# Optimization experiments

Hardware: AMD Instinct MI355X
Metric: run time of the kernel (lower is better)

The kernel has to match this reference:

```python
import jax, jax.numpy as jnp
import numpy as np

B, T, V, H = 2048, 48, 59, 512


def _uniform(key, shape, fan_in):
    stdv = 1.0 / np.sqrt(fan_in)
    return jax.random.uniform(key, shape, jnp.float32, -stdv, stdv)


def setup_inputs() -> dict:
    key = jax.random.key(0)
    ks = jax.random.split(key, 24)
    x = jax.random.normal(ks[0], (B, T, V), jnp.float32)
    mask = (jax.random.uniform(ks[1], (B, T, V)) < 0.8).astype(jnp.float32)
    deltas = jax.random.uniform(ks[2], (B, T, V), jnp.float32)
    return {
        "x": x, "mask": mask, "deltas": deltas,
        # Decay h (temp_decay_h): W [H,V], b [H]
        "W_gh": _uniform(ks[3], (H, V), V), "b_gh": _uniform(ks[4], (H,), V),
        # Decay x (diag): only diagonal of [V,V] is used -> store diag [V]
        "w_gx": _uniform(ks[5], (V,), V), "b_gx": _uniform(ks[6], (V,), V),
        # hist: Linear(H -> V)
        "W_hist": _uniform(ks[7], (V, H), H), "b_hist": _uniform(ks[8], (V,), H),
        "W_fr": _uniform(ks[9], (V, V), V), "b_fr": _uniform(ks[10], (V,), V),
        # weight_combine: Linear(2V -> V)
        "W_wc": _uniform(ks[11], (V, 2 * V), 2 * V), "b_wc": _uniform(ks[12], (V,), 2 * V),
        # LSTMCell(2V -> H), torch gate order i,f,g,o
        "W_ih": _uniform(ks[13], (4 * H, 2 * V), 2 * V),
        "W_hh": _uniform(ks[14], (4 * H, H), H),
        "b_ih": _uniform(ks[15], (4 * H,), H),
        "b_hh": _uniform(ks[16], (4 * H,), H),
    }


def _rits_forward(x, mask, deltas, W_gh, b_gh, w_gx, b_gx, W_hist, b_hist,
                  W_fr, b_fr, W_wc, b_wc, W_ih, W_hh, b_ih, b_hh):
    Bb, Tt, Vv = x.shape
    Hh = W_gh.shape[0]
    offdiag = 1.0 - jnp.eye(Vv, dtype=x.dtype)
    W_fr_m = W_fr * offdiag

    def step(carry, inp):
        h, c, loss = carry
        x_t, m_t, d_t = inp  # each [B, V]
        # temporal decay of hidden state
        gamma_h = jnp.exp(-jax.nn.relu(d_t @ W_gh.T + b_gh))  # [B, H]
        h = h * gamma_h
        # history-based estimate
        x_h = h @ W_hist.T + b_hist  # [B, V]
        x_r = m_t * x_t + (1.0 - m_t) * x_h
        xu = x_r @ W_fr_m.T + b_fr  # [B, V]
        # diagonal input decay
        gamma_x = jnp.exp(-jax.nn.relu(d_t * w_gx + b_gx))  # [B, V]
        # combination weights (note: no sigmoid, faithful to source)
        beta = jnp.concatenate([gamma_x, m_t], axis=-1) @ W_wc.T + b_wc  # [B, V]
        x_comb = beta * xu + (1.0 - beta) * x_h
        loss = loss + jnp.sum(jnp.abs(x_t - x_comb) * m_t) / (jnp.sum(m_t) + 1e-5)
        x_imp_t = m_t * x_t + (1.0 - m_t) * x_comb
        # LSTM cell
        inp_t = jnp.concatenate([x_imp_t, m_t], axis=-1)  # [B, 2V]
        gates = inp_t @ W_ih.T + b_ih + h @ W_hh.T + b_hh  # [B, 4H]
        i_g, f_g, g_g, o_g = jnp.split(gates, 4, axis=-1)
        c = jax.nn.sigmoid(f_g) * c + jax.nn.sigmoid(i_g) * jnp.tanh(g_g)
        h = jax.nn.sigmoid(o_g) * jnp.tanh(c)
        return (h, c, loss), (x_imp_t, h)

    h0 = jnp.zeros((Bb, Hh), x.dtype)
    c0 = jnp.zeros((Bb, Hh), x.dtype)
    loss0 = jnp.zeros((), x.dtype)
    xs = (jnp.swapaxes(x, 0, 1), jnp.swapaxes(mask, 0, 1), jnp.swapaxes(deltas, 0, 1))
    (h, c, x_loss), (x_imp_t, hiddens_t) = jax.lax.scan(step, (h0, c0, loss0), xs)
    x_imp = jnp.swapaxes(x_imp_t, 0, 1)      # [B, T, V]
    hiddens = jnp.swapaxes(hiddens_t, 0, 1)  # [B, T, H]
    return x_imp, x_loss, hiddens


def reference(x, mask, deltas, W_gh, b_gh, w_gx, b_gx, W_hist, b_hist,
              W_fr, b_fr, W_wc, b_wc, W_ih, W_hh, b_ih, b_hh):
    return _rits_forward(x, mask, deltas, W_gh, b_gh, w_gx, b_gx, W_hist, b_hist,
                         W_fr, b_fr, W_wc, b_wc, W_ih, W_hh, b_ih, b_hh)
```

## Files before the change

### kernel.cpp

```cpp
#include <hip/hip_runtime.h>

#define B_ 2048
#define T_ 48
#define V_ 59
#define H_ 512
#define KP_ 640
#define G4_ 2048

typedef __bf16 bf16x8 __attribute__((ext_vector_type(8)));
typedef float f32x4 __attribute__((ext_vector_type(4)));

__device__ __forceinline__ unsigned short f2bf(float x){
  union { float f; unsigned u; } v; v.f = x;
  unsigned r = (v.u + 0x7FFFu + ((v.u >> 16) & 1u)) >> 16;
  return (unsigned short)r;
}
__device__ __forceinline__ float sigf(float x){ return 1.f/(1.f+expf(-x)); }

static const size_t OFF_Hws = 0;
static const size_t OFF_Cws = 4194304;
static const size_t OFF_LN  = 8388608;
static const size_t OFF_LD  = OFF_LN + 256;
static const size_t MEMSET_BYTES = OFF_LN + 512;
static const size_t OFF_A   = OFF_LN + 512;
static const size_t OFF_WGT = OFF_A  + (size_t)B_*KP_*2;
static const size_t OFF_WGH = OFF_WGT + (size_t)G4_*KP_*2;
static const size_t OFF_WHB = OFF_WGH + 120832;
static const size_t OFF_WFR = OFF_WHB + 120832;
static const size_t OFF_WWC = OFF_WFR + 14080;

__global__ void init_k(const float* __restrict__ W_gh, const float* __restrict__ W_hist,
                       const float* __restrict__ W_fr, const float* __restrict__ W_wc,
                       const float* __restrict__ W_ih, const float* __restrict__ W_hh,
                       float* __restrict__ WghT, unsigned short* __restrict__ WhB,
                       float* __restrict__ WfrT, float* __restrict__ WwcT,
                       unsigned short* __restrict__ WgT, unsigned short* __restrict__ A_buf)
{
  int tid = blockIdx.x*blockDim.x + threadIdx.x;
  int nt  = gridDim.x*blockDim.x;
  for (int i = tid; i < V_*H_; i += nt){ int v = i >> 9, j = i & 511; WghT[i] = W_gh[j*V_ + v]; }
  for (int i = tid; i < 64*H_; i += nt){ int n = i >> 9; WhB[i] = (n < V_) ? f2bf(W_hist[i]) : (unsigned short)0; }
  for (int i = tid; i < V_*V_; i += nt){ int u = i / V_, v = i - u*V_; WfrT[i] = (u==v) ? 0.f : W_fr[v*V_ + u]; }
  for (int i = tid; i < 2*V_*V_; i += nt){ int u = i / V_, v = i - u*V_; WwcT[i] = W_wc[v*(2*V_) + u]; }
  for (int i = tid; i < G4_*KP_; i += nt){
    int n = i / KP_, k = i - n*KP_;
    float v = 0.f;
    if (k < 2*V_)      v = W_ih[n*(2*V_) + k];
    else if (k < 630)  v = W_hh[n*H_ + (k-118)];
    WgT[i] = f2bf(v);
  }
  for (int i = tid; i < B_*10; i += nt){ int b = i / 10, p = i - b*10; A_buf[(size_t)b*KP_ + 630 + p] = 0; }
}

__global__ __launch_bounds__(512) void phase1(int t,
    const float* __restrict__ x, const float* __restrict__ mk, const float* __restrict__ dl,
    const float* __restrict__ b_gh, const float* __restrict__ w_gx, const float* __restrict__ b_gx,
    const float* __restrict__ b_hist, const float* __restrict__ b_fr, const float* __restrict__ b_wc,
    const float* __restrict__ WghT, const unsigned short* __restrict__ WhB,
    const float* __restrict__ WfrT, const float* __restrict__ WwcT,
    const float* __restrict__ h_ws, unsigned short* __restrict__ A_buf,
    float* __restrict__ out_ximp, float* __restrict__ loss_num, float* __restrict__ loss_den)
{
  __shared__ float d_s[8*64], m_s[8*64], x_s[8*64];
  __shared__ float xh_s[8*64], xr_s[8*64], gx_s[8*64];
  __shared__ unsigned short hA[16*520];
  __shared__ float red[16];
  const int tid = threadIdx.x;
  const int r1  = blockIdx.x * 8;

  if (tid < 8*V_) {
    int b = tid / V_, v = tid - b*V_;
    size_t g = ((size_t)(r1+b)*T_ + t)*V_ + v;
    d_s[b*64+v] = dl[g];
    m_s[b*64+v] = mk[g];
    x_s[b*64+v] = x[g];
  }
  __syncthreads();

  {
    int j = tid;
    float acc[8];
#pragma unroll
    for (int b=0;b<8;++b) acc[b]=0.f;
    for (int v=0; v<V_; ++v) {
      float wv = WghT[v*H_ + j];
#pragma unroll
      for (int b=0;b<8;++b) acc[b] += d_s[b*64+v]*wv;
    }
    float bg = b_gh[j];
#pragma unroll
    for (int b=0;b<8;++b) {
      float gh = expf(-fmaxf(acc[b]+bg, 0.f));
      float hv = h_ws[(size_t)(r1+b)*H_ + j] * gh;
      unsigned short hb = f2bf(hv);
      hA[b*520 + j] = hb;
      A_buf[(size_t)(r1+b)*KP_ + 118 + j] = hb;
    }
  }
  __syncthreads();

  if (tid < 256) {
    const int w = tid >> 6, lane = tid & 63, col = lane & 15, quad = lane >> 4;
    f32x4 acc = (f32x4)(0.f);
    const unsigned short* wb = WhB + (size_t)(w*16 + col)*H_;
#pragma unroll
    for (int kk = 0; kk < 16; ++kk) {
      bf16x8 a  = *reinterpret_cast<const bf16x8*>(&hA[col*520 + kk*32 + quad*8]);
      bf16x8 bb = *reinterpret_cast<const bf16x8*>(wb + kk*32 + quad*8);
      acc = __builtin_amdgcn_mfma_f32_16x16x32_bf16(a, bb, acc, 0, 0, 0);
    }
    if (quad < 2) {
      int v = w*16 + col;
      float bh = (v < V_) ? b_hist[v] : 0.f;
#pragma unroll
      for (int r=0; r<4; ++r) xh_s[(quad*4+r)*64 + v] = acc[r] + bh;
    }
  } else {
    for (int i = tid - 256; i < 512; i += 256) {
      int b = i >> 6, v = i & 63;
      if (v < V_) {
        float mm = m_s[b*64+v], dd = d_s[b*64+v];
        gx_s[b*64+v] = expf(-fmaxf(dd*w_gx[v]+b_gx[v], 0.f));
        A_buf[(size_t)(r1+b)*KP_ + V_ + v] = f2bf(mm);
      }
    }
  }
  __syncthreads();

  {
    int b = tid>>6, v = tid&63;
    if (v < V_) {
      float mm = m_s[b*64+v];
      xr_s[b*64+v] = mm*x_s[b*64+v] + (1.f-mm)*xh_s[b*64+v];
    }
  }
  __syncthreads();

  float num = 0.f, den = 0.f;
  {
    int b = tid>>6, v = tid&63;
    if (v < V_) {
      float xu = b_fr[v], bt = b_wc[v];
      for (int u=0; u<V_; ++u) {
        xu += xr_s[b*64+u]*WfrT[u*V_+v];
        bt += gx_s[b*64+u]*WwcT[u*V_+v] + m_s[b*64+u]*WwcT[(V_+u)*V_+v];
      }
      float xh = xh_s[b*64+v];
      float xc = bt*xu + (1.f-bt)*xh;
      float mm = m_s[b*64+v], xx = x_s[b*64+v];
      num = fabsf(xx - xc)*mm;
      den = mm;
      float xi = mm*xx + (1.f-mm)*xc;
      out_ximp[((size_t)(r1+b)*T_ + t)*V_ + v] = xi;
      A_buf[(size_t)(r1+b)*KP_ + v] = f2bf(xi);
    }
  }
#pragma unroll
  for (int off=32; off; off>>=1){ num += __shfl_down(num, off); den += __shfl_down(den, off); }
  int wid = tid>>6, lane = tid&63;
  if (lane == 0){ red[wid] = num; red[8+wid] = den; }
  __syncthreads();
  if (tid == 0){
    float n=0.f, d=0.f;
    for (int i=0;i<8;++i){ n += red[i]; d += red[8+i]; }
    atomicAdd(&loss_num[t], n);
    atomicAdd(&loss_den[t], d);
  }
}

__global__ __launch_bounds__(512) void phase2(int t,
    const unsigned short* __restrict__ A_buf, const unsigned short* __restrict__ WgT,
    const float* __restrict__ b_ih, const float* __restrict__ b_hh,
    float* __restrict__ h_ws, float* __restrict__ c_ws, float* __restrict__ out_hid)
{
  __shared__ uint4 ldsA[128*8];
  __shared__ uint4 ldsB[128*8];
  const int tid  = threadIdx.x;
  const int r0   = blockIdx.x * 128;
  const int j0   = blockIdx.y * 32;
  const int w    = tid >> 6;
  const int rg   = w >> 1;
  const int uh   = w & 1;
  const int lane = tid & 63;
  const int col  = lane & 15;
  const int quad = lane >> 4;

  f32x4 acc[2][4];
#pragma unroll
  for (int i=0;i<2;++i)
#pragma unroll
    for (int g=0;g<4;++g) acc[i][g] = (f32x4)(0.f);

  for (int s = 0; s < 10; ++s) {
#pragma unroll
    for (int p=0; p<2; ++p) {
      int idx = p*512 + tid;
      int r = idx >> 3, c = idx & 7;
      ldsA[r*8 + (c ^ (r&7))] = *reinterpret_cast<const uint4*>(A_buf + (size_t)(r0+r)*KP_ + s*64 + c*8);
      int ng = ((r>>5)<<9) + j0 + (r&31);
      ldsB[r*8 + (c ^ (r&7))] = *reinterpret_cast<const uint4*>(WgT + (size_t)ng*KP_ + s*64 + c*8);
    }
    __syncthreads();
#pragma unroll
    for (int kk=0; kk<2; ++kk) {
      bf16x8 af[2], bfr[4];
#pragma unroll
      for (int mf=0; mf<2; ++mf) {
        int r = rg*32 + mf*16 + col;
        af[mf] = *reinterpret_cast<const bf16x8*>(&ldsA[r*8 + ((kk*4+quad) ^ (r&7))]);
      }
#pragma unroll
      for (int g=0; g<4; ++g) {
        int r = g*32 + uh*16 + col;
        bfr[g] = *reinterpret_cast<const bf16x8*>(&ldsB[r*8 + ((kk*4+quad) ^ (r&7))]);
      }
#pragma unroll
      for (int mf=0; mf<2; ++mf)
#pragma unroll
        for (int g=0; g<4; ++g)
          acc[mf][g] = __builtin_amdgcn_mfma_f32_16x16x32_bf16(af[mf], bfr[g], acc[mf][g], 0, 0, 0);
    }
    __syncthreads();
  }

  {
    int u = j0 + uh*16 + col;
    float bi  = b_ih[u]        + b_hh[u];
    float bf_ = b_ih[H_+u]     + b_hh[H_+u];
    float bg  = b_ih[2*H_+u]   + b_hh[2*H_+u];
    float bo  = b_ih[3*H_+u]   + b_hh[3*H_+u];
#pragma unroll
    for (int mf=0; mf<2; ++mf) {
#pragma unroll
      for (int r=0; r<4; ++r) {
        int b = r0 + rg*32 + mf*16 + quad*4 + r;
        float gi = acc[mf][0][r] + bi;
        float gf = acc[mf][1][r] + bf_;
        float gg = acc[mf][2][r] + bg;
        float go = acc[mf][3][r] + bo;
        size_t idx = (size_t)b*H_ + u;
        float co = c_ws[idx];
        float cn = sigf(gf)*co + sigf(gi)*tanhf(gg);
        float hn = sigf(go)*tanhf(cn);
        c_ws[idx] = cn;
        h_ws[idx] = hn;
        out_hid[((size_t)b*T_ + t)*H_ + u] = hn;
      }
    }
  }
}

__global__ void loss_k(const float* __restrict__ loss_num, const float* __restrict__ loss_den,
                       float* __restrict__ out_loss)
{
  int tid = threadIdx.x;
  float v = 0.f;
  if (tid < T_) v = loss_num[tid]/(loss_den[tid] + 1e-5f);
#pragma unroll
  for (int off=32; off; off>>=1) v += __shfl_down(v, off);
  if (tid == 0) *out_loss = v;
}

extern "C" void kernel_launch(void* const* d_in, const int* in_sizes, int n_in,
                              void* d_out, int out_size, void* d_ws, size_t ws_size,
                              hipStream_t stream)
{
  const float* x      = (const float*)d_in[0];
  const float* mk     = (const float*)d_in[1];
  const float* dl     = (const float*)d_in[2];
  const float* W_gh   = (const float*)d_in[3];
  const float* b_gh   = (const float*)d_in[4];
  const float* w_gx   = (const float*)d_in[5];
  const float* b_gx   = (const float*)d_in[6];
  const float* W_hist = (const float*)d_in[7];
  const float* b_hist = (const float*)d_in[8];
  const float* W_fr   = (const float*)d_in[9];
  const float* b_fr   = (const float*)d_in[10];
  const float* W_wc   = (const float*)d_in[11];
  const float* b_wc   = (const float*)d_in[12];
  const float* W_ih   = (const float*)d_in[13];
  const float* W_hh   = (const float*)d_in[14];
  const float* b_ih   = (const float*)d_in[15];
  const float* b_hh   = (const float*)d_in[16];

  char* ws = (char*)d_ws;
  float*          h_ws   = (float*)(ws + OFF_Hws);
  float*          c_ws   = (float*)(ws + OFF_Cws);
  float*          lnum   = (float*)(ws + OFF_LN);
  float*          lden   = (float*)(ws + OFF_LD);
  unsigned short* A_buf  = (unsigned short*)(ws + OFF_A);
  unsigned short* WgT    = (unsigned short*)(ws + OFF_WGT);
  float*          WghT   = (float*)(ws + OFF_WGH);
  unsigned short* WhB    = (unsigned short*)(ws + OFF_WHB);
  float*          WfrT   = (float*)(ws + OFF_WFR);
  float*          WwcT   = (float*)(ws + OFF_WWC);

  float* out      = (float*)d_out;
  float* out_ximp = out;
  float* out_loss = out + (size_t)B_*T_*V_;
  float* out_hid  = out + (size_t)B_*T_*V_ + 1;

  hipMemsetAsync(d_ws, 0, MEMSET_BYTES, stream);
  init_k<<<1024, 256, 0, stream>>>(W_gh, W_hist, W_fr, W_wc, W_ih, W_hh,
                                   WghT, WhB, WfrT, WwcT, WgT, A_buf);
  for (int t = 0; t < T_; ++t) {
    phase1<<<256, 512, 0, stream>>>(t, x, mk, dl, b_gh, w_gx, b_gx, b_hist, b_fr, b_wc,
                                    WghT, WhB, WfrT, WwcT, h_ws, A_buf,
                                    out_ximp, lnum, lden);
    phase2<<<dim3(16,16), 512, 0, stream>>>(t, A_buf, WgT, b_ih, b_hh,
                                            h_ws, c_ws, out_hid);
  }
  loss_k<<<1, 64, 0, stream>>>(lnum, lden, out_loss);
}
```

Before: 2.363 ms.

## Fuse per-step kernels into one persistent kernel with grid barriers; precompute beta

Replaces the 96 per-timestep kernel launches with a single persistent kernel of 256 blocks. The blocks synchronise through an atomic-counter grid barrier between the input-imputation phase and the LSTM GEMM phase. The cell state now stays in registers instead of global memory. The weight-combine beta term, which does not depend on the recurrence, is computed for all timesteps up front in a separate parallel kernel, along with the loss denominators. The design relies on all 256 blocks being resident at once, and spin barriers add their own latency in exchange for removing launch overhead.

Measured after the change: 5.006 ms. 112% more time.

```diff
diff --git a/kernel.cpp b/kernel.cpp
--- a/kernel.cpp
+++ b/kernel.cpp
@@ -6,6 +6,7 @@
 #define H_ 512
 #define KP_ 640
 #define G4_ 2048
+#define NBLK_ 256
 
 typedef __bf16 bf16x8 __attribute__((ext_vector_type(8)));
 typedef float f32x4 __attribute__((ext_vector_type(4)));
@@ -17,23 +18,23 @@
 }
 __device__ __forceinline__ float sigf(float x){ return 1.f/(1.f+expf(-x)); }
 
-static const size_t OFF_Hws = 0;
-static const size_t OFF_Cws = 4194304;
-static const size_t OFF_LN  = 8388608;
-static const size_t OFF_LD  = OFF_LN + 256;
-static const size_t MEMSET_BYTES = OFF_LN + 512;
-static const size_t OFF_A   = OFF_LN + 512;
-static const size_t OFF_WGT = OFF_A  + (size_t)B_*KP_*2;
-static const size_t OFF_WGH = OFF_WGT + (size_t)G4_*KP_*2;
-static const size_t OFF_WHB = OFF_WGH + 120832;
-static const size_t OFF_WFR = OFF_WHB + 120832;
-static const size_t OFF_WWC = OFF_WFR + 14080;
+static const size_t OFF_H    = 0;
+static const size_t OFF_LN   = 4194304;
+static const size_t OFF_LD   = OFF_LN + 256;
+static const size_t OFF_CNT  = OFF_LD + 256;
+static const size_t MEMSET_BYTES = OFF_CNT + 256;
+static const size_t OFF_A    = MEMSET_BYTES;
+static const size_t OFF_WGT  = OFF_A + (size_t)B_*KP_*2;
+static const size_t OFF_WGH  = OFF_WGT + (size_t)G4_*KP_*2;
+static const size_t OFF_WHB  = OFF_WGH + 120832;
+static const size_t OFF_WFR  = OFF_WHB + 65536;
+static const size_t OFF_BETA = OFF_WFR + 14080;
 
 __global__ void init_k(const float* __restrict__ W_gh, const float* __restrict__ W_hist,
-                       const float* __restrict__ W_fr, const float* __restrict__ W_wc,
+                       const float* __restrict__ W_fr,
                        const float* __restrict__ W_ih, const float* __restrict__ W_hh,
                        float* __restrict__ WghT, unsigned short* __restrict__ WhB,
-                       float* __restrict__ WfrT, float* __restrict__ WwcT,
+                       float* __restrict__ WfrT,
                        unsigned short* __restrict__ WgT, unsigned short* __restrict__ A_buf)
 {
   int tid = blockIdx.x*blockDim.x + threadIdx.x;
@@ -41,7 +42,6 @@
   for (int i = tid; i < V_*H_; i += nt){ int v = i >> 9, j = i & 511; WghT[i] = W_gh[j*V_ + v]; }
   for (int i = tid; i < 64*H_; i += nt){ int n = i >> 9; WhB[i] = (n < V_) ? f2bf(W_hist[i]) : (unsigned short)0; }
   for (int i = tid; i < V_*V_; i += nt){ int u = i / V_, v = i - u*V_; WfrT[i] = (u==v) ? 0.f : W_fr[v*V_ + u]; }
-  for (int i = tid; i < 2*V_*V_; i += nt){ int u = i / V_, v = i - u*V_; WwcT[i] = W_wc[v*(2*V_) + u]; }
   for (int i = tid; i < G4_*KP_; i += nt){
     int n = i / KP_, k = i - n*KP_;
     float v = 0.f;
@@ -52,213 +52,258 @@
   for (int i = tid; i < B_*10; i += nt){ int b = i / 10, p = i - b*10; A_buf[(size_t)b*KP_ + 630 + p] = 0; }
 }
 
-__global__ __launch_bounds__(512) void phase1(int t,
+__global__ __launch_bounds__(256) void beta_k(
+    const float* __restrict__ mk, const float* __restrict__ dl,
+    const float* __restrict__ w_gx, const float* __restrict__ b_gx,
+    const float* __restrict__ W_wc, const float* __restrict__ b_wc,
+    float* __restrict__ beta_pre, float* __restrict__ loss_den)
+{
+  __shared__ float gx[4][64], mm[4][64];
+  const int tid = threadIdx.x;
+  const int rw  = tid >> 6, v = tid & 63;
+  const int row = blockIdx.x*4 + rw;
+  size_t base = (size_t)row * V_;
+  float m = 0.f, g = 0.f;
+  if (v < V_){
+    float d = dl[base+v];
+    m = mk[base+v];
+    g = expf(-fmaxf(d*w_gx[v]+b_gx[v], 0.f));
+  }
+  gx[rw][v] = g; mm[rw][v] = m;
+  __syncthreads();
+  if (v < V_){
+    float bt = b_wc[v];
+    const float* wr = W_wc + (size_t)v*(2*V_);
+    for (int u = 0; u < V_; ++u)
+      bt += gx[rw][u]*wr[u] + mm[rw][u]*wr[V_+u];
+    beta_pre[base+v] = bt;
+  }
+  float s = m;
+#pragma unroll
+  for (int off=32; off; off>>=1) s += __shfl_down(s, off);
+  if (v == 0){
+    int t = row % T_;
+    atomicAdd(&loss_den[t], s);
+  }
+}
+
+__device__ __forceinline__ void grid_bar(unsigned int* cnt, unsigned int target){
+  __syncthreads();
+  if (threadIdx.x == 0){
+    __threadfence();
+    __hip_atomic_fetch_add(cnt, 1u, __ATOMIC_RELEASE, __HIP_MEMORY_SCOPE_AGENT);
+    while (__hip_atomic_load(cnt, __ATOMIC_RELAXED, __HIP_MEMORY_SCOPE_AGENT) < target)
+      __builtin_amdgcn_s_sleep(1);
+    __threadfence();
+  }
+  __syncthreads();
+}
+
+__global__ __launch_bounds__(512) void fused(
     const float* __restrict__ x, const float* __restrict__ mk, const float* __restrict__ dl,
-    const float* __restrict__ b_gh, const float* __restrict__ w_gx, const float* __restrict__ b_gx,
-    const float* __restrict__ b_hist, const float* __restrict__ b_fr, const float* __restrict__ b_wc,
+    const float* __restrict__ b_gh, const float* __restrict__ b_hist, const float* __restrict__ b_fr,
     const float* __restrict__ WghT, const unsigned short* __restrict__ WhB,
-    const float* __restrict__ WfrT, const float* __restrict__ WwcT,
-    const float* __restrict__ h_ws, unsigned short* __restrict__ A_buf,
-    float* __restrict__ out_ximp, float* __restrict__ loss_num, float* __restrict__ loss_den)
+    const float* __restrict__ WfrT, const float* __restrict__ beta_pre,
+    const unsigned short* __restrict__ WgT,
+    const float* __restrict__ b_ih, const float* __restrict__ b_hh,
+    float* h_ws, unsigned short* A_buf, unsigned int* bar_cnt,
+    float* loss_num, const float* __restrict__ loss_den,
+    float* __restrict__ out_ximp, float* __restrict__ out_hid, float* __restrict__ out_loss)
 {
-  __shared__ float d_s[8*64], m_s[8*64], x_s[8*64];
-  __shared__ float xh_s[8*64], xr_s[8*64], gx_s[8*64];
-  __shared__ unsigned short hA[16*520];
-  __shared__ float red[16];
-  const int tid = threadIdx.x;
-  const int r1  = blockIdx.x * 8;
-
-  if (tid < 8*V_) {
-    int b = tid / V_, v = tid - b*V_;
-    size_t g = ((size_t)(r1+b)*T_ + t)*V_ + v;
-    d_s[b*64+v] = dl[g];
-    m_s[b*64+v] = mk[g];
-    x_s[b*64+v] = x[g];
-  }
-  __syncthreads();
-
-  {
-    int j = tid;
-    float acc[8];
-#pragma unroll
-    for (int b=0;b<8;++b) acc[b]=0.f;
-    for (int v=0; v<V_; ++v) {
-      float wv = WghT[v*H_ + j];
-#pragma unroll
-      for (int b=0;b<8;++b) acc[b] += d_s[b*64+v]*wv;
-    }
-    float bg = b_gh[j];
-#pragma unroll
-    for (int b=0;b<8;++b) {
-      float gh = expf(-fmaxf(acc[b]+bg, 0.f));
-      float hv = h_ws[(size_t)(r1+b)*H_ + j] * gh;
-      unsigned short hb = f2bf(hv);
-      hA[b*520 + j] = hb;
-      A_buf[(size_t)(r1+b)*KP_ + 118 + j] = hb;
-    }
-  }
-  __syncthreads();
-
-  if (tid < 256) {
-    const int w = tid >> 6, lane = tid & 63, col = lane & 15, quad = lane >> 4;
-    f32x4 acc = (f32x4)(0.f);
-    const unsigned short* wb = WhB + (size_t)(w*16 + col)*H_;
-#pragma unroll
-    for (int kk = 0; kk < 16; ++kk) {
-      bf16x8 a  = *reinterpret_cast<const bf16x8*>(&hA[col*520 + kk*32 + quad*8]);
-      bf16x8 bb = *reinterpret_cast<const bf16x8*>(wb + kk*32 + quad*8);
-      acc = __builtin_amdgcn_mfma_f32_16x16x32_bf16(a, bb, acc, 0, 0, 0);
-    }
-    if (quad < 2) {
-      int v = w*16 + col;
-      float bh = (v < V_) ? b_hist[v] : 0.f;
-#pragma unroll
-      for (int r=0; r<4; ++r) xh_s[(quad*4+r)*64 + v] = acc[r] + bh;
-    }
-  } else {
-    for (int i = tid - 256; i < 512; i += 256) {
-      int b = i >> 6, v = i & 63;
-      if (v < V_) {
-        float mm = m_s[b*64+v], dd = d_s[b*64+v];
-        gx_s[b*64+v] = expf(-fmaxf(dd*w_gx[v]+b_gx[v], 0.f));
-        A_buf[(size_t)(r1+b)*KP_ + V_ + v] = f2bf(mm);
-      }
-    }
-  }
-  __syncthreads();
-
-  {
-    int b = tid>>6, v = tid&63;
-    if (v < V_) {
-      float mm = m_s[b*64+v];
-      xr_s[b*64+v] = mm*x_s[b*64+v] + (1.f-mm)*xh_s[b*64+v];
-    }
-  }
-  __syncthreads();
-
-  float num = 0.f, den = 0.f;
-  {
-    int b = tid>>6, v = tid&63;
-    if (v < V_) {
-      float xu = b_fr[v], bt = b_wc[v];
-      for (int u=0; u<V_; ++u) {
-        xu += xr_s[b*64+u]*WfrT[u*V_+v];
-        bt += gx_s[b*64+u]*WwcT[u*V_+v] + m_s[b*64+u]*WwcT[(V_+u)*V_+v];
-      }
-      float xh = xh_s[b*64+v];
-      float xc = bt*xu + (1.f-bt)*xh;
-      float mm = m_s[b*64+v], xx = x_s[b*64+v];
-      num = fabsf(xx - xc)*mm;
-      den = mm;
-      float xi = mm*xx + (1.f-mm)*xc;
-      out_ximp[((size_t)(r1+b)*T_ + t)*V_ + v] = xi;
-      A_buf[(size_t)(r1+b)*KP_ + v] = f2bf(xi);
-    }
-  }
-#pragma unroll
-  for (int off=32; off; off>>=1){ num += __shfl_down(num, off); den += __shfl_down(den, off); }
-  int wid = tid>>6, lane = tid&63;
-  if (lane == 0){ red[wid] = num; red[8+wid] = den; }
-  __syncthreads();
-  if (tid == 0){
-    float n=0.f, d=0.f;
-    for (int i=0;i<8;++i){ n += red[i]; d += red[8+i]; }
-    atomicAdd(&loss_num[t], n);
-    atomicAdd(&loss_den[t], d);
-  }
-}
-
-__global__ __launch_bounds__(512) void phase2(int t,
-    const unsigned short* __restrict__ A_buf, const unsigned short* __restrict__ WgT,
-    const float* __restrict__ b_ih, const float* __restrict__ b_hh,
-    float* __restrict__ h_ws, float* __restrict__ c_ws, float* __restrict__ out_hid)
-{
-  __shared__ uint4 ldsA[128*8];
-  __shared__ uint4 ldsB[128*8];
+  __shared__ union {
+    struct {
+      float d_s[512], m_s[512], x_s[512], xh_s[512], xr_s[512];
+      unsigned short hA[16*520];
+      float red[8];
+    } p1;
+    struct { uint4 sA[1024]; uint4 sB[1024]; } p2;
+  } sm;
+
   const int tid  = threadIdx.x;
-  const int r0   = blockIdx.x * 128;
-  const int j0   = blockIdx.y * 32;
-  const int w    = tid >> 6;
-  const int rg   = w >> 1;
-  const int uh   = w & 1;
+  const int blk  = blockIdx.x;
+  const int r1   = blk * 8;
+  const int r0   = (blk & 15) * 128;
+  const int j0   = (blk >> 4) * 32;
+  const int wid  = tid >> 6;
   const int lane = tid & 63;
   const int col  = lane & 15;
   const int quad = lane >> 4;
-
-  f32x4 acc[2][4];
+  const int rg   = wid >> 1;
+  const int uh   = wid & 1;
+
+  const int u2 = j0 + uh*16 + col;
+  const float bi  = b_ih[u2]      + b_hh[u2];
+  const float bfg = b_ih[H_+u2]   + b_hh[H_+u2];
+  const float bgg = b_ih[2*H_+u2] + b_hh[2*H_+u2];
+  const float bog = b_ih[3*H_+u2] + b_hh[3*H_+u2];
+  const float bgj = b_gh[tid];
+
+  float creg[2][4];
 #pragma unroll
   for (int i=0;i<2;++i)
 #pragma unroll
-    for (int g=0;g<4;++g) acc[i][g] = (f32x4)(0.f);
-
-  for (int s = 0; s < 10; ++s) {
-#pragma unroll
-    for (int p=0; p<2; ++p) {
-      int idx = p*512 + tid;
-      int r = idx >> 3, c = idx & 7;
-      ldsA[r*8 + (c ^ (r&7))] = *reinterpret_cast<const uint4*>(A_buf + (size_t)(r0+r)*KP_ + s*64 + c*8);
-      int ng = ((r>>5)<<9) + j0 + (r&31);
-      ldsB[r*8 + (c ^ (r&7))] = *reinterpret_cast<const uint4*>(WgT + (size_t)ng*KP_ + s*64 + c*8);
-    }
-    __syncthreads();
-#pragma unroll
-    for (int kk=0; kk<2; ++kk) {
-      bf16x8 af[2], bfr[4];
-#pragma unroll
-      for (int mf=0; mf<2; ++mf) {
-        int r = rg*32 + mf*16 + col;
-        af[mf] = *reinterpret_cast<const bf16x8*>(&ldsA[r*8 + ((kk*4+quad) ^ (r&7))]);
-      }
-#pragma unroll
-      for (int g=0; g<4; ++g) {
-        int r = g*32 + uh*16 + col;
-        bfr[g] = *reinterpret_cast<const bf16x8*>(&ldsB[r*8 + ((kk*4+quad) ^ (r&7))]);
-      }
-#pragma unroll
-      for (int mf=0; mf<2; ++mf)
-#pragma unroll
-        for (int g=0; g<4; ++g)
-          acc[mf][g] = __builtin_amdgcn_mfma_f32_16x16x32_bf16(af[mf], bfr[g], acc[mf][g], 0, 0, 0);
-    }
-    __syncthreads();
-  }
-
-  {
-    int u = j0 + uh*16 + col;
-    float bi  = b_ih[u]        + b_hh[u];
-    float bf_ = b_ih[H_+u]     + b_hh[H_+u];
-    float bg  = b_ih[2*H_+u]   + b_hh[2*H_+u];
-    float bo  = b_ih[3*H_+u]   + b_hh[3*H_+u];
-#pragma unroll
-    for (int mf=0; mf<2; ++mf) {
-#pragma unroll
-      for (int r=0; r<4; ++r) {
-        int b = r0 + rg*32 + mf*16 + quad*4 + r;
-        float gi = acc[mf][0][r] + bi;
-        float gf = acc[mf][1][r] + bf_;
-        float gg = acc[mf][2][r] + bg;
-        float go = acc[mf][3][r] + bo;
-        size_t idx = (size_t)b*H_ + u;
-        float co = c_ws[idx];
-        float cn = sigf(gf)*co + sigf(gi)*tanhf(gg);
-        float hn = sigf(go)*tanhf(cn);
-        c_ws[idx] = cn;
-        h_ws[idx] = hn;
-        out_hid[((size_t)b*T_ + t)*H_ + u] = hn;
-      }
-    }
-  }
-}
-
-__global__ void loss_k(const float* __restrict__ loss_num, const float* __restrict__ loss_den,
-                       float* __restrict__ out_loss)
-{
-  int tid = threadIdx.x;
-  float v = 0.f;
-  if (tid < T_) v = loss_num[tid]/(loss_den[tid] + 1e-5f);
-#pragma unroll
-  for (int off=32; off; off>>=1) v += __shfl_down(v, off);
-  if (tid == 0) *out_loss = v;
+    for (int r=0;r<4;++r) creg[i][r] = 0.f;
+
+  unsigned int tgt = 0;
+
+  for (int t = 0; t < T_; ++t){
+    if (tid < 8*V_){
+      int b = tid / V_, v = tid - b*V_;
+      size_t g = ((size_t)(r1+b)*T_ + t)*V_ + v;
+      sm.p1.d_s[b*64+v] = dl[g];
+      sm.p1.m_s[b*64+v] = mk[g];
+      sm.p1.x_s[b*64+v] = x[g];
+    }
+    __syncthreads();
+
+    {
+      float acc[8];
+#pragma unroll
+      for (int b=0;b<8;++b) acc[b]=0.f;
+      for (int v=0; v<V_; ++v){
+        float wv = WghT[v*H_ + tid];
+#pragma unroll
+        for (int b=0;b<8;++b) acc[b] += sm.p1.d_s[b*64+v]*wv;
+      }
+#pragma unroll
+      for (int b=0;b<8;++b){
+        float gh = expf(-fmaxf(acc[b]+bgj, 0.f));
+        float hv = h_ws[(size_t)(r1+b)*H_ + tid] * gh;
+        unsigned short hb = f2bf(hv);
+        sm.p1.hA[b*520 + tid] = hb;
+        A_buf[(size_t)(r1+b)*KP_ + 118 + tid] = hb;
+      }
+    }
+    __syncthreads();
+
+    if (tid < 256){
+      f32x4 acc = (f32x4)(0.f);
+      const unsigned short* wb = WhB + (size_t)(wid*16 + col)*H_;
+#pragma unroll
+      for (int kk = 0; kk < 16; ++kk){
+        bf16x8 a  = *reinterpret_cast<const bf16x8*>(&sm.p1.hA[col*520 + kk*32 + quad*8]);
+        bf16x8 bb = *reinterpret_cast<const bf16x8*>(wb + kk*32 + quad*8);
+        acc = __builtin_amdgcn_mfma_f32_16x16x32_bf16(a, bb, acc, 0, 0, 0);
+      }
+      if (quad < 2){
+        int v = wid*16 + col;
+        float bh = (v < V_) ? b_hist[v] : 0.f;
+#pragma unroll
+        for (int r=0;r<4;++r) sm.p1.xh_s[(quad*4+r)*64 + v] = acc[r] + bh;
+      }
+    } else {
+      for (int i = tid - 256; i < 512; i += 256){
+        int b = i >> 6, v = i & 63;
+        if (v < V_) A_buf[(size_t)(r1+b)*KP_ + V_ + v] = f2bf(sm.p1.m_s[b*64+v]);
+      }
+    }
+    __syncthreads();
+
+    {
+      int b = wid, v = lane;
+      if (v < V_){
+        float mm2 = sm.p1.m_s[b*64+v];
+        sm.p1.xr_s[b*64+v] = mm2*sm.p1.x_s[b*64+v] + (1.f-mm2)*sm.p1.xh_s[b*64+v];
+      }
+    }
+    __syncthreads();
+
+    float num = 0.f;
+    {
+      int b = wid, v = lane;
+      if (v < V_){
+        float xu = b_fr[v];
+        for (int u=0; u<V_; ++u) xu += sm.p1.xr_s[b*64+u]*WfrT[u*V_+v];
+        float bt = beta_pre[((size_t)(r1+b)*T_ + t)*V_ + v];
+        float xh = sm.p1.xh_s[b*64+v];
+        float xc = bt*xu + (1.f-bt)*xh;
+        float mm2 = sm.p1.m_s[b*64+v], xx = sm.p1.x_s[b*64+v];
+        num = fabsf(xx - xc)*mm2;
+        float xi = mm2*xx + (1.f-mm2)*xc;
+        out_ximp[((size_t)(r1+b)*T_ + t)*V_ + v] = xi;
+        A_buf[(size_t)(r1+b)*KP_ + v] = f2bf(xi);
+      }
+    }
+#pragma unroll
+    for (int off=32; off; off>>=1) num += __shfl_down(num, off);
+    if (lane == 0) sm.p1.red[wid] = num;
+    __syncthreads();
+    if (tid == 0){
+      float n = 0.f;
+#pragma unroll
+      for (int i=0;i<8;++i) n += sm.p1.red[i];
+      atomicAdd(&loss_num[t], n);
+    }
+
+    grid_bar(bar_cnt, tgt += NBLK_);
+
+    f32x4 acc2[2][4];
+#pragma unroll
+    for (int i=0;i<2;++i)
+#pragma unroll
+      for (int g=0;g<4;++g) acc2[i][g] = (f32x4)(0.f);
+
+    for (int s = 0; s < 10; ++s){
+#pragma unroll
+      for (int p=0; p<2; ++p){
+        int idx = p*512 + tid;
+        int r = idx >> 3, c = idx & 7;
+        sm.p2.sA[r*8 + (c ^ (r&7))] = *reinterpret_cast<const uint4*>(A_buf + (size_t)(r0+r)*KP_ + s*64 + c*8);
+        int ng = ((r>>5)<<9) + j0 + (r&31);
+        sm.p2.sB[r*8 + (c ^ (r&7))] = *reinterpret_cast<const uint4*>(WgT + (size_t)ng*KP_ + s*64 + c*8);
+      }
+      __syncthreads();
+#pragma unroll
+      for (int kk=0; kk<2; ++kk){
+        bf16x8 af[2], bfr[4];
+#pragma unroll
+        for (int mf=0; mf<2; ++mf){
+          int r = rg*32 + mf*16 + col;
+          af[mf] = *reinterpret_cast<const bf16x8*>(&sm.p2.sA[r*8 + ((kk*4+quad) ^ (r&7))]);
+        }
+#pragma unroll
+        for (int g=0; g<4; ++g){
+          int r = g*32 + uh*16 + col;
+          bfr[g] = *reinterpret_cast<const bf16x8*>(&sm.p2.sB[r*8 + ((kk*4+quad) ^ (r&7))]);
+        }
+#pragma unroll
+        for (int mf=0; mf<2; ++mf)
+#pragma unroll
+          for (int g=0; g<4; ++g)
+            acc2[mf][g] = __builtin_amdgcn_mfma_f32_16x16x32_bf16(af[mf], bfr[g], acc2[mf][g], 0, 0, 0);
+      }
+      __syncthreads();
+    }
+
+    {
+#pragma unroll
+      for (int mf=0; mf<2; ++mf){
+#pragma unroll
+        for (int r=0; r<4; ++r){
+          int b = r0 + rg*32 + mf*16 + quad*4 + r;
+          float gi = acc2[mf][0][r] + bi;
+          float gf = acc2[mf][1][r] + bfg;
+          float gg = acc2[mf][2][r] + bgg;
+          float go = acc2[mf][3][r] + bog;
+          float cn = sigf(gf)*creg[mf][r] + sigf(gi)*tanhf(gg);
+          float hn = sigf(go)*tanhf(cn);
+          creg[mf][r] = cn;
+          h_ws[(size_t)b*H_ + u2] = hn;
+          out_hid[((size_t)b*T_ + t)*H_ + u2] = hn;
+        }
+      }
+    }
+
+    grid_bar(bar_cnt, tgt += NBLK_);
+  }
+
+  if (blk == 0 && tid < 64){
+    float v = 0.f;
+    if (tid < T_) v = loss_num[tid]/(loss_den[tid] + 1e-5f);
+#pragma unroll
+    for (int off=32; off; off>>=1) v += __shfl_down(v, off);
+    if (tid == 0) *out_loss = v;
+  }
 }
 
 extern "C" void kernel_launch(void* const* d_in, const int* in_sizes, int n_in,
@@ -284,16 +329,16 @@
   const float* b_hh   = (const float*)d_in[16];
 
   char* ws = (char*)d_ws;
-  float*          h_ws   = (float*)(ws + OFF_Hws);
-  float*          c_ws   = (float*)(ws + OFF_Cws);
+  float*          h_ws   = (float*)(ws + OFF_H);
   float*          lnum   = (float*)(ws + OFF_LN);
   float*          lden   = (float*)(ws + OFF_LD);
+  unsigned int*   cnt    = (unsigned int*)(ws + OFF_CNT);
   unsigned short* A_buf  = (unsigned short*)(ws + OFF_A);
   unsigned short* WgT    = (unsigned short*)(ws + OFF_WGT);
   float*          WghT   = (float*)(ws + OFF_WGH);
   unsigned short* WhB    = (unsigned short*)(ws + OFF_WHB);
   float*          WfrT   = (float*)(ws + OFF_WFR);
-  float*          WwcT   = (float*)(ws + OFF_WWC);
+  float*          beta   = (float*)(ws + OFF_BETA);
 
   float* out      = (float*)d_out;
   float* out_ximp = out;
@@ -301,14 +346,11 @@
   float* out_hid  = out + (size_t)B_*T_*V_ + 1;
 
   hipMemsetAsync(d_ws, 0, MEMSET_BYTES, stream);
-  init_k<<<1024, 256, 0, stream>>>(W_gh, W_hist, W_fr, W_wc, W_ih, W_hh,
-                                   WghT, WhB, WfrT, WwcT, WgT, A_buf);
-  for (int t = 0; t < T_; ++t) {
-    phase1<<<256, 512, 0, stream>>>(t, x, mk, dl, b_gh, w_gx, b_gx, b_hist, b_fr, b_wc,
-                                    WghT, WhB, WfrT, WwcT, h_ws, A_buf,
-                                    out_ximp, lnum, lden);
-    phase2<<<dim3(16,16), 512, 0, stream>>>(t, A_buf, WgT, b_ih, b_hh,
-                                            h_ws, c_ws, out_hid);
-  }
-  loss_k<<<1, 64, 0, stream>>>(lnum, lden, out_loss);
-}
+  init_k<<<1024, 256, 0, stream>>>(W_gh, W_hist, W_fr, W_ih, W_hh,
+                                   WghT, WhB, WfrT, WgT, A_buf);
+  beta_k<<<(B_*T_)/4, 256, 0, stream>>>(mk, dl, w_gx, b_gx, W_wc, b_wc, beta, lden);
+  fused<<<NBLK_, 512, 0, stream>>>(x, mk, dl, b_gh, b_hist, b_fr,
+                                   WghT, WhB, WfrT, beta, WgT, b_ih, b_hh,
+                                   h_ws, A_buf, cnt, lnum, lden,
+                                   out_ximp, out_hid, out_loss);
+}
```
